# Optimization experiments

Hardware: AMD Instinct MI355X
Metric: run time of the kernel (lower is better)

## Reference

```python
import jax, jax.numpy as jnp
import numpy as np

HEADS = 8
# (src_type, dst_type) for the 8 edge types; node types: 0=op, 1=machine, 2=job
EDGE_DEFS = ((2, 0), (0, 2), (0, 0), (0, 0), (0, 1), (0, 1), (1, 0), (1, 0))
EPS = 1e-5


def _graph_norm(x, gamma, beta):
    # PyG LayerNorm(mode='graph') with batch=None: normalize over ALL nodes and features
    mu = x.mean()
    std = jnp.sqrt(((x - mu) ** 2).mean())
    return (x - mu) / (std + EPS) * gamma + beta


def _hgt_layer(xs, edges, Wkqv, bkqv, krel, vrel, prel, Wout, bout, skip):
    h = xs[0].shape[-1]
    D = h // HEADS
    Ns = [int(x.shape[0]) for x in xs]
    off = np.concatenate([[0], np.cumsum(Ns)])
    Ntot = int(off[-1])
    k, q, v = [], [], []
    for t, x in enumerate(xs):
        kqv = x @ Wkqv[t] + bkqv[t]                    # [N_t, 3h]
        kt, qt, vt = jnp.split(kqv, 3, axis=1)
        k.append(kt.reshape(-1, HEADS, D))
        q.append(qt.reshape(-1, HEADS, D))
        v.append(vt.reshape(-1, HEADS, D))
    alphas, msgs, idxs = [], [], []
    for e, (s, d) in enumerate(EDGE_DEFS):
        src, dst = edges[e][0], edges[e][1]
        # per-edge-type relation transform applied per source node, then gathered per edge
        ke = jnp.einsum('nhd,hde->nhe', k[s], krel[e])[src]   # [E, H, D]
        ve = jnp.einsum('nhd,hde->nhe', v[s], vrel[e])[src]   # [E, H, D]
        qe = q[d][dst]                                        # [E, H, D]
        a = (qe * ke).sum(-1) * prel[e] / jnp.sqrt(jnp.asarray(D, qe.dtype))  # [E, H]
        alphas.append(a)
        msgs.append(ve)
        idxs.append(dst + int(off[d]))
    alpha = jnp.concatenate(alphas, 0)
    msg = jnp.concatenate(msgs, 0)
    idx = jnp.concatenate(idxs, 0)
    # segment softmax over ALL incoming edges per (type-offset) destination node
    amax = jax.ops.segment_max(alpha, idx, num_segments=Ntot)
    ex = jnp.exp(alpha - amax[idx])
    den = jax.ops.segment_sum(ex, idx, num_segments=Ntot)
    w = ex / den[idx]
    agg = jax.ops.segment_sum(msg * w[..., None], idx, num_segments=Ntot).reshape(Ntot, h)
    outs = []
    for t in range(3):
        o = jax.nn.gelu(agg[off[t]:off[t + 1]], approximate=False) @ Wout[t] + bout[t]
        g = jax.nn.sigmoid(skip[t])
        outs.append(g * o + (1.0 - g) * xs[t])
    return outs


def _forward(op_x, machine_x, job_x, W_op, b_op, W_mach, b_mach, W_job, b_job,
             ln_gamma, ln_beta, Wkqv, bkqv, krel, vrel, prel, Wout, bout, skip,
             Wp1, bp1, Wp2, bp2, Wp3, bp3, Wv1, bv1, Wv2, bv2,
             edges, op_idx, m_idx):
    xs = [
        _graph_norm(op_x @ W_op + b_op, ln_gamma[0], ln_beta[0]),
        _graph_norm(machine_x @ W_mach + b_mach, ln_gamma[1], ln_beta[1]),
        _graph_norm(job_x @ W_job + b_job, ln_gamma[2], ln_beta[2]),
    ]
    for l in range(Wkqv.shape[0]):
        xs = _hgt_layer(xs, edges, Wkqv[l], bkqv[l], krel[l], vrel[l], prel[l],
                        Wout[l], bout[l], skip[l])
    op_e, mach_e, job_e = xs
    g = jnp.concatenate([op_e.mean(0), mach_e.mean(0), job_e.mean(0)])  # [3h] global pooled
    value = (jax.nn.relu(g @ Wv1 + bv1) @ Wv2 + bv2)[0]
    P = op_idx.shape[0]
    z = jnp.concatenate([op_e[op_idx], mach_e[m_idx],
                         jnp.broadcast_to(g, (P, g.shape[0]))], axis=1)   # [P, 5h]
    z = jax.nn.relu(z @ Wp1 + bp1)
    z = jax.nn.relu(z @ Wp2 + bp2)
    logits = (z @ Wp3 + bp3)[:, 0]
    return logits, value


def setup_inputs() -> dict:
    key = jax.random.key(0)
    ks = iter(jax.random.split(key, 64))
    NOP, NM, NJ = 50_000, 1_000, 5_000
    H, L, P = 64, 2, 20_000
    D = H // HEADS
    OPF, MF, JF = 8, 7, 7

    def nrm(shape, scale):
        return jax.random.normal(next(ks), shape, jnp.float32) * scale

    def edge(n_src, n_dst, E):
        src = jax.random.randint(next(ks), (E,), 0, n_src, jnp.int32)
        dst = jax.random.randint(next(ks), (E,), 0, n_dst, jnp.int32)
        return jnp.stack([src, dst])

    return {
        'op_x': nrm((NOP, OPF), 1.0),
        'machine_x': nrm((NM, MF), 1.0),
        'job_x': nrm((NJ, JF), 1.0),
        'W_op': nrm((OPF, H), OPF ** -0.5), 'b_op': jnp.zeros((H,), jnp.float32),
        'W_mach': nrm((MF, H), MF ** -0.5), 'b_mach': jnp.zeros((H,), jnp.float32),
        'W_job': nrm((JF, H), JF ** -0.5), 'b_job': jnp.zeros((H,), jnp.float32),
        'ln_gamma': jnp.ones((3, H), jnp.float32), 'ln_beta': jnp.zeros((3, H), jnp.float32),
        'Wkqv': nrm((L, 3, H, 3 * H), H ** -0.5), 'bkqv': jnp.zeros((L, 3, 3 * H), jnp.float32),
        'krel': nrm((L, 8, HEADS, D, D), D ** -0.5), 'vrel': nrm((L, 8, HEADS, D, D), D ** -0.5),
        'prel': jnp.ones((L, 8, HEADS), jnp.float32),
        'Wout': nrm((L, 3, H, H), H ** -0.5), 'bout': jnp.zeros((L, 3, H), jnp.float32),
        'skip': jnp.ones((L, 3), jnp.float32),
        'Wp1': nrm((5 * H, H), (5 * H) ** -0.5), 'bp1': jnp.zeros((H,), jnp.float32),
        'Wp2': nrm((H, H // 2), H ** -0.5), 'bp2': jnp.zeros((H // 2,), jnp.float32),
        'Wp3': nrm((H // 2, 1), (H // 2) ** -0.5), 'bp3': jnp.zeros((1,), jnp.float32),
        'Wv1': nrm((3 * H, H), (3 * H) ** -0.5), 'bv1': jnp.zeros((H,), jnp.float32),
        'Wv2': nrm((H, 1), H ** -0.5), 'bv2': jnp.zeros((1,), jnp.float32),
        'e_contains': edge(NJ, NOP, 50_000),
        'e_belongs': edge(NOP, NJ, 50_000),
        'e_prec': edge(NOP, NOP, 50_000),
        'e_mprec': edge(NOP, NOP, 50_000),
        'e_onmach': edge(NOP, NM, 50_000),
        'e_assign': edge(NOP, NM, 50_000),
        'e_canproc': edge(NM, NOP, 150_000),
        'e_proc': edge(NM, NOP, 50_000),
        'op_idx': jax.random.randint(next(ks), (P,), 0, NOP, jnp.int32),
        'm_idx': jax.random.randint(next(ks), (P,), 0, NM, jnp.int32),
    }


def reference(op_x, machine_x, job_x, W_op, b_op, W_mach, b_mach, W_job, b_job,
              ln_gamma, ln_beta, Wkqv, bkqv, krel, vrel, prel, Wout, bout, skip,
              Wp1, bp1, Wp2, bp2, Wp3, bp3, Wv1, bv1, Wv2, bv2,
              e_contains, e_belongs, e_prec, e_mprec, e_onmach, e_assign,
              e_canproc, e_proc, op_idx, m_idx):
    edges = (e_contains, e_belongs, e_prec, e_mprec, e_onmach, e_assign, e_canproc, e_proc)
    return _forward(op_x, machine_x, job_x, W_op, b_op, W_mach, b_mach, W_job, b_job,
                    ln_gamma, ln_beta, Wkqv, bkqv, krel, vrel, prel, Wout, bout, skip,
                    Wp1, bp1, Wp2, bp2, Wp3, bp3, Wv1, bv1, Wv2, bv2,
                    edges, op_idx, m_idx)
```

## Files before the change

### kernel.cpp

```cpp
#include <hip/hip_runtime.h>


#define KT 32
#define OT 64

__global__ void k_zero2(unsigned int* __restrict__ a, int na,
                        unsigned int* __restrict__ b, int nb) {
    int i = blockIdx.x * 256 + threadIdx.x;
    int st = gridDim.x * 256;
    int tot = na + nb;
    for (; i < tot; i += st) {
        if (i < na) a[i] = 0u; else b[i - na] = 0u;
    }
}

__global__ void k_build(const int* __restrict__ p0, const int* __restrict__ p1,
                        const int* __restrict__ p2, const int* __restrict__ p3,
                        const int* __restrict__ p4, const int* __restrict__ p5,
                        const int* __restrict__ p6, const int* __restrict__ p7,
                        int c1, int c2, int c3, int c4, int c5, int c6, int c7, int c8,
                        int* __restrict__ gkey, int* __restrict__ pack,
                        int* __restrict__ cnt, int fb,
                        const float* __restrict__ op_x, const float* __restrict__ mach_x,
                        const float* __restrict__ job_x,
                        const float* __restrict__ W_op, const float* __restrict__ b_op,
                        const float* __restrict__ W_mach, const float* __restrict__ b_mach,
                        const float* __restrict__ W_job, const float* __restrict__ b_job,
                        float* __restrict__ X, float* __restrict__ nacc,
                        int N0, int N1, int N2) {
    if (blockIdx.x < fb) {
        int g = blockIdx.x * 256 + threadIdx.x;
        if (g >= c8) return;
        const int* ep; int base, E0, et, soff, doff;
        int OJ = N0 + N1;
        if (g < c1)      { ep = p0; base = 0;  E0 = c1 - 0;  et = 0; soff = OJ;  doff = 0;  }
        else if (g < c2) { ep = p1; base = c1; E0 = c2 - c1; et = 1; soff = 0;   doff = OJ; }
        else if (g < c3) { ep = p2; base = c2; E0 = c3 - c2; et = 2; soff = 0;   doff = 0;  }
        else if (g < c4) { ep = p3; base = c3; E0 = c4 - c3; et = 3; soff = 0;   doff = 0;  }
        else if (g < c5) { ep = p4; base = c4; E0 = c5 - c4; et = 4; soff = 0;   doff = N0; }
        else if (g < c6) { ep = p5; base = c5; E0 = c6 - c5; et = 5; soff = 0;   doff = N0; }
        else if (g < c7) { ep = p6; base = c6; E0 = c7 - c6; et = 6; soff = N0;  doff = 0;  }
        else             { ep = p7; base = c7; E0 = c8 - c7; et = 7; soff = N0;  doff = 0;  }
        int i = g - base;
        int kd = (ep[E0 + i] + doff) * 8 + et;
        gkey[g] = kd;
        pack[g] = ep[i] + soff;
        atomicAdd(&cnt[kd], 1);
        return;
    }
    int bid = blockIdx.x - fb;
    int tid = threadIdx.x;
    int j = tid & 63, w = tid >> 6;
    float w0[8], w1[7], w2[7];
    for (int k = 0; k < 8; k++) w0[k] = W_op[k * 64 + j];
    for (int k = 0; k < 7; k++) w1[k] = W_mach[k * 64 + j];
    for (int k = 0; k < 7; k++) w2[k] = W_job[k * 64 + j];
    float b0 = b_op[j], b1 = b_mach[j], b2 = b_job[j];
    float s10 = 0, s20 = 0, s11 = 0, s21 = 0, s12 = 0, s22 = 0;
    int Ntot = N0 + N1 + N2;
    for (int n = bid * 4 + w; n < Ntot; n += 512 * 4) {
        float a;
        if (n < N0) {
            const float* xr = op_x + (size_t)n * 8;
            a = b0;
            for (int k = 0; k < 8; k++) a += xr[k] * w0[k];
            s10 += a; s20 += a * a;
        } else if (n < N0 + N1) {
            const float* xr = mach_x + (size_t)(n - N0) * 7;
            a = b1;
            for (int k = 0; k < 7; k++) a += xr[k] * w1[k];
            s11 += a; s21 += a * a;
        } else {
            const float* xr = job_x + (size_t)(n - N0 - N1) * 7;
            a = b2;
            for (int k = 0; k < 7; k++) a += xr[k] * w2[k];
            s12 += a; s22 += a * a;
        }
        X[(size_t)n * 64 + j] = a;
    }
    for (int o = 32; o > 0; o >>= 1) {
        s10 += __shfl_down(s10, o); s20 += __shfl_down(s20, o);
        s11 += __shfl_down(s11, o); s21 += __shfl_down(s21, o);
        s12 += __shfl_down(s12, o); s22 += __shfl_down(s22, o);
    }
    __shared__ float r[4][6];
    if (j == 0) {
        r[w][0] = s10; r[w][1] = s20; r[w][2] = s11;
        r[w][3] = s21; r[w][4] = s12; r[w][5] = s22;
    }
    __syncthreads();
    if (tid < 6) {
        float v = r[0][tid] + r[1][tid] + r[2][tid] + r[3][tid];
        atomicAdd(&nacc[tid], v);
    }
}

__global__ void k_scan1(const int* __restrict__ cnt, int* __restrict__ partial, int M) {
    __shared__ int s[256];
    int t = threadIdx.x;
    int i = blockIdx.x * 256 + t;
    s[t] = (i < M) ? cnt[i] : 0;
    __syncthreads();
    for (int o = 128; o > 0; o >>= 1) {
        if (t < o) s[t] += s[t + o];
        __syncthreads();
    }
    if (t == 0) partial[blockIdx.x] = s[0];
}

__global__ void k_scan2(const int* __restrict__ cnt, const int* __restrict__ partial,
                        int* __restrict__ rowptr8, int* __restrict__ cursor,
                        int M, int Etot) {
    __shared__ int s[256];
    __shared__ int pbase;
    int t = threadIdx.x;
    int ps = 0;
    for (int c = t; c < blockIdx.x; c += 256) ps += partial[c];
    s[t] = ps;
    __syncthreads();
    for (int o = 128; o > 0; o >>= 1) {
        if (t < o) s[t] += s[t + o];
        __syncthreads();
    }
    if (t == 0) pbase = s[0];
    __syncthreads();
    int base = pbase;
    int i = blockIdx.x * 256 + t;
    int v = (i < M) ? cnt[i] : 0;
    s[t] = v;
    __syncthreads();
    for (int off = 1; off < 256; off <<= 1) {
        int add = (t >= off) ? s[t - off] : 0;
        __syncthreads();
        s[t] += add;
        __syncthreads();
    }
    if (i < M) {
        int r = base + s[t] - v;
        rowptr8[i] = r;
        cursor[i] = r;
    }
    if (blockIdx.x == 0 && t == 0) rowptr8[M] = Etot;
}

__global__ void k_scatter(const int* __restrict__ gkey, const int* __restrict__ pack,
                          int* __restrict__ cursor, int* __restrict__ csr, int Etot) {
    int i = blockIdx.x * 256 + threadIdx.x;
    if (i >= Etot) return;
    int d = gkey[i];
    int pos = atomicAdd(&cursor[d], 1);
    csr[pos] = pack[i];
}

__global__ void k_kqvT(float* __restrict__ X, const float* __restrict__ nacc,
                       const float* __restrict__ ln_gamma, const float* __restrict__ ln_beta,
                       const float* __restrict__ Wl, const float* __restrict__ bl,
                       float* __restrict__ KQV, int tb0, int tb1,
                       int N0, int N1, int N2, int do_norm) {
    __shared__ float Ws[64 * 192];
    __shared__ float Xs[64 * 36];
    __shared__ float Bs[192];
    int b = blockIdx.x;
    int t, nbase, Nt, chunk;
    if (b < tb0)            { t = 0; chunk = b;             nbase = 0;       Nt = N0; }
    else if (b < tb0 + tb1) { t = 1; chunk = b - tb0;       nbase = N0;      Nt = N1; }
    else                    { t = 2; chunk = b - tb0 - tb1; nbase = N0 + N1; Nt = N2; }
    int n0 = nbase + chunk * KT;
    int cntm = nbase + Nt - n0; if (cntm > KT) cntm = KT;

    int tid = threadIdx.x;
    const float* W = Wl + (size_t)t * 64 * 192;
    for (int i = tid; i < 64 * 192; i += 192) Ws[i] = W[i];
    Bs[tid] = bl[t * 192 + tid];

    float mu = 0.0f, sc = 0.0f;
    if (do_norm) {
        float inv = 1.0f / ((float)Nt * 64.0f);
        mu = nacc[2 * t] * inv;
        float var = nacc[2 * t + 1] * inv - mu * mu;
        sc = 1.0f / (sqrtf(fmaxf(var, 0.0f)) + 1e-5f);
    }
    for (int idx = tid; idx < KT * 64; idx += 192) {
        int m = idx >> 6, k = idx & 63;
        float v = 0.0f;
        if (m < cntm) {
            v = X[(size_t)(n0 + m) * 64 + k];
            if (do_norm) {
                v = (v - mu) * sc * ln_gamma[t * 64 + k] + ln_beta[t * 64 + k];
                X[(size_t)(n0 + m) * 64 + k] = v;
            }
        }
        Xs[k * 36 + m] = v;
    }
    __syncthreads();

    int c = tid;
    float bc = Bs[c];
    float acc[KT];
#pragma unroll
    for (int m = 0; m < KT; m++) acc[m] = bc;
    for (int k = 0; k < 64; k++) {
        float wv = Ws[k * 192 + c];
        const float4* xr = (const float4*)(Xs + k * 36);
#pragma unroll
        for (int q = 0; q < KT / 4; q++) {
            float4 x4 = xr[q];
            acc[q * 4 + 0] += x4.x * wv;
            acc[q * 4 + 1] += x4.y * wv;
            acc[q * 4 + 2] += x4.z * wv;
            acc[q * 4 + 3] += x4.w * wv;
        }
    }
    for (int m = 0; m < cntm; m++)
        KQV[(size_t)(n0 + m) * 192 + c] = acc[m];
}

__global__ void k_attnagg(const float* __restrict__ KQV, const int* __restrict__ csr,
                          const int* __restrict__ rowptr8,
                          const float* __restrict__ krel_l, const float* __restrict__ vrel_l,
                          const float* __restrict__ prel_l, float* __restrict__ agg, int Ntot) {
    __shared__ float KRs[8 * 8 * 72];
    __shared__ float VRs[8 * 8 * 72];
    int tid = threadIdx.x;
    for (int i = tid; i < 4096; i += 512) {
        int eth = i >> 6, rest = i & 63;
        KRs[eth * 72 + rest] = krel_l[i] * (prel_l[eth] * 0.35355339059327373f);
        VRs[eth * 72 + rest] = vrel_l[i];
    }
    __syncthreads();

    int j = tid & 63, h = j >> 3, ee = j & 7;
    int wave  = blockIdx.x * 8 + (tid >> 6);
    int nwave = gridDim.x * 8;
    for (int n = wave; n < Ntot; n += nwave) {
        float qv = KQV[(size_t)n * 192 + 64 + j];
        float num = 0.0f, den = 0.0f;
        int e0 = rowptr8[n * 8];
        for (int et = 0; et < 8; et++) {
            int e1 = rowptr8[n * 8 + et + 1];
            if (e0 < e1) {
                const float* KR = KRs + (et * 8 + h) * 72 + ee;
                const float* VR = VRs + (et * 8 + h) * 72 + ee;
                float kr0 = KR[0],  kr1 = KR[8],  kr2 = KR[16], kr3 = KR[24];
                float kr4 = KR[32], kr5 = KR[40], kr6 = KR[48], kr7 = KR[56];
                float vr0 = VR[0],  vr1 = VR[8],  vr2 = VR[16], vr3 = VR[24];
                float vr4 = VR[32], vr5 = VR[40], vr6 = VR[48], vr7 = VR[56];
                int idx = e0;
                for (; idx + 2 <= e1; idx += 2) {
                    int sn0 = csr[idx], sn1 = csr[idx + 1];
                    const float4* ka = (const float4*)(KQV + (size_t)sn0 * 192 + h * 8);
                    const float4* va = (const float4*)(KQV + (size_t)sn0 * 192 + 128 + h * 8);
                    const float4* kb = (const float4*)(KQV + (size_t)sn1 * 192 + h * 8);
                    const float4* vb = (const float4*)(KQV + (size_t)sn1 * 192 + 128 + h * 8);
                    float4 a0 = ka[0], a1 = ka[1], av0 = va[0], av1 = va[1];
                    float4 b0 = kb[0], b1 = kb[1], bv0 = vb[0], bv1 = vb[1];
                    float ke0 = a0.x * kr0 + a0.y * kr1 + a0.z * kr2 + a0.w * kr3
                              + a1.x * kr4 + a1.y * kr5 + a1.z * kr6 + a1.w * kr7;
                    float ve0 = av0.x * vr0 + av0.y * vr1 + av0.z * vr2 + av0.w * vr3
                              + av1.x * vr4 + av1.y * vr5 + av1.z * vr6 + av1.w * vr7;
                    float ke1 = b0.x * kr0 + b0.y * kr1 + b0.z * kr2 + b0.w * kr3
                              + b1.x * kr4 + b1.y * kr5 + b1.z * kr6 + b1.w * kr7;
                    float ve1 = bv0.x * vr0 + bv0.y * vr1 + bv0.z * vr2 + bv0.w * vr3
                              + bv1.x * vr4 + bv1.y * vr5 + bv1.z * vr6 + bv1.w * vr7;
                    float t0 = qv * ke0;
                    t0 += __shfl_xor(t0, 1); t0 += __shfl_xor(t0, 2); t0 += __shfl_xor(t0, 4);
                    float t1 = qv * ke1;
                    t1 += __shfl_xor(t1, 1); t1 += __shfl_xor(t1, 2); t1 += __shfl_xor(t1, 4);
                    float ex0 = __expf(t0);
                    float ex1 = __expf(t1);
                    num += ex0 * ve0 + ex1 * ve1;
                    den += ex0 + ex1;
                }
                if (idx < e1) {
                    int sn = csr[idx];
                    const float4* kr4p = (const float4*)(KQV + (size_t)sn * 192 + h * 8);
                    const float4* vr4p = (const float4*)(KQV + (size_t)sn * 192 + 128 + h * 8);
                    float4 k0 = kr4p[0], k1 = kr4p[1], v0 = vr4p[0], v1 = vr4p[1];
                    float ke = k0.x * kr0 + k0.y * kr1 + k0.z * kr2 + k0.w * kr3
                             + k1.x * kr4 + k1.y * kr5 + k1.z * kr6 + k1.w * kr7;
                    float ve = v0.x * vr0 + v0.y * vr1 + v0.z * vr2 + v0.w * vr3
                             + v1.x * vr4 + v1.y * vr5 + v1.z * vr6 + v1.w * vr7;
                    float tq = qv * ke;
                    tq += __shfl_xor(tq, 1); tq += __shfl_xor(tq, 2); tq += __shfl_xor(tq, 4);
                    float ex = __expf(tq);
                    num += ex * ve;
                    den += ex;
                }
            }
            e0 = e1;
        }
        agg[(size_t)n * 64 + j] = (den > 0.0f) ? (num / den) : 0.0f;
    }
}

__global__ void k_outT(const float* __restrict__ agg, float* __restrict__ X,
                       const float* __restrict__ Wl, const float* __restrict__ bl,
                       const float* __restrict__ skipl, float* __restrict__ gsum,
                       int tb0, int tb1, int N0, int N1, int N2, int do_pool) {
    __shared__ float Ws[64 * 64];
    __shared__ float Gs[64 * 68];
    int b = blockIdx.x;
    int t, nbase, Nt, chunk;
    if (b < tb0)            { t = 0; chunk = b;             nbase = 0;       Nt = N0; }
    else if (b < tb0 + tb1) { t = 1; chunk = b - tb0;       nbase = N0;      Nt = N1; }
    else                    { t = 2; chunk = b - tb0 - tb1; nbase = N0 + N1; Nt = N2; }
    int n0 = nbase + chunk * OT;
    int cntm = nbase + Nt - n0; if (cntm > OT) cntm = OT;

    int tid = threadIdx.x;
    const float* W = Wl + (size_t)t * 64 * 64;
    for (int i = tid; i < 4096; i += 256) Ws[i] = W[i];
    for (int idx = tid; idx < OT * 64; idx += 256) {
        int m = idx >> 6, k = idx & 63;
        float v = 0.0f;
        if (m < cntm) {
            float x = agg[(size_t)(n0 + m) * 64 + k];
            v = 0.5f * x * (1.0f + erff(x * 0.70710678118654752f));
        }
        Gs[k * 68 + m] = v;
    }
    __syncthreads();

    int c = tid & 63, w = tid >> 6;
    float bc = bl[t * 64 + c];
    float gk = 1.0f / (1.0f + __expf(-skipl[t]));
    int m0 = w * 16;
    float acc[16];
#pragma unroll
    for (int i = 0; i < 16; i++) acc[i] = bc;
    for (int k = 0; k < 64; k++) {
        float wv = Ws[k * 64 + c];
        const float4* gr = (const float4*)(Gs + k * 68 + m0);
#pragma unroll
        for (int q = 0; q < 4; q++) {
            float4 g4 = gr[q];
            acc[q * 4 + 0] += g4.x * wv;
            acc[q * 4 + 1] += g4.y * wv;
            acc[q * 4 + 2] += g4.z * wv;
            acc[q * 4 + 3] += g4.w * wv;
        }
    }
    float psum = 0.0f;
    for (int i = 0; i < 16; i++) {
        int m = m0 + i;
        if (m < cntm) {
            float xold = X[(size_t)(n0 + m) * 64 + c];
            float xn = gk * acc[i] + (1.0f - gk) * xold;
            X[(size_t)(n0 + m) * 64 + c] = xn;
            psum += xn;
        }
    }
    if (do_pool) {
        __syncthreads();
        Gs[w * 64 + c] = psum;
        __syncthreads();
        if (tid < 64) {
            float tot = Gs[c] + Gs[64 + c] + Gs[128 + c] + Gs[192 + c];
            atomicAdd(&gsum[t * 64 + c], tot);
        }
    }
}

__global__ void HGTPolicy_53051436040798_kernel(
        const float* __restrict__ X, const float* __restrict__ gsum,
        const int* __restrict__ op_idx, const int* __restrict__ m_idx,
        const float* __restrict__ Wp1, const float* __restrict__ bp1,
        const float* __restrict__ Wp2, const float* __restrict__ bp2,
        const float* __restrict__ Wp3, const float* __restrict__ bp3,
        const float* __restrict__ Wv1, const float* __restrict__ bv1,
        const float* __restrict__ Wv2, const float* __restrict__ bv2,
        float* __restrict__ out, int N0, int N1, int N2, int P, int nb) {
    int tid = threadIdx.x;
    if (blockIdx.x == nb) {
        __shared__ float g[192];
        __shared__ float h1[64];
        int j = tid;
        if (j < 192) {
            float Nd = (j < 64) ? (float)N0 : ((j < 128) ? (float)N1 : (float)N2);
            g[j] = gsum[j] / Nd;
        }
        __syncthreads();
        if (j < 64) {
            float a = bv1[j];
            for (int k = 0; k < 192; k++) a += g[k] * Wv1[k * 64 + j];
            h1[j] = fmaxf(a, 0.0f);
        }
        __syncthreads();
        if (j == 0) {
            float v = bv2[0];
            for (int k = 0; k < 64; k++) v += h1[k] * Wv2[k];
            out[P] = v;
        }
        return;
    }
    __shared__ float z[8][320];
    __shared__ float h1p[8][64];
    __shared__ float h2p[8][32];
    int pp = tid >> 6, j = tid & 63;
    int p = blockIdx.x * 8 + pp;
    int valid = (p < P);
    if (valid) {
        int on = op_idx[p], mn = m_idx[p];
        z[pp][j]       = X[(size_t)on * 64 + j];
        z[pp][64 + j]  = X[(size_t)(N0 + mn) * 64 + j];
        z[pp][128 + j] = gsum[j] / (float)N0;
        z[pp][192 + j] = gsum[64 + j] / (float)N1;
        z[pp][256 + j] = gsum[128 + j] / (float)N2;
    }
    __syncthreads();
    if (valid) {
        const float* zp = z[pp];
        float a = bp1[j];
        for (int k = 0; k < 320; k++) a += zp[k] * Wp1[k * 64 + j];
        h1p[pp][j] = fmaxf(a, 0.0f);
    }
    __syncthreads();
    if (valid && j < 32) {
        const float* hp = h1p[pp];
        float a2 = bp2[j];
        for (int k = 0; k < 64; k++) a2 += hp[k] * Wp2[k * 32 + j];
        h2p[pp][j] = fmaxf(a2, 0.0f);
    }
    __syncthreads();
    if (valid && j == 0) {
        const float* hp = h2p[pp];
        float lg = bp3[0];
        for (int k = 0; k < 32; k++) lg += hp[k] * Wp3[k];
        out[p] = lg;
    }
}

extern "C" void kernel_launch(void* const* d_in, const int* in_sizes, int n_in,
                              void* d_out, int out_size, void* d_ws, size_t ws_size,
                              hipStream_t stream) {
    const float* op_x      = (const float*)d_in[0];
    const float* machine_x = (const float*)d_in[1];
    const float* job_x     = (const float*)d_in[2];
    const float* W_op   = (const float*)d_in[3];
    const float* b_op   = (const float*)d_in[4];
    const float* W_mach = (const float*)d_in[5];
    const float* b_mach = (const float*)d_in[6];
    const float* W_job  = (const float*)d_in[7];
    const float* b_job  = (const float*)d_in[8];
    const float* ln_gamma = (const float*)d_in[9];
    const float* ln_beta  = (const float*)d_in[10];
    const float* Wkqv = (const float*)d_in[11];
    const float* bkqv = (const float*)d_in[12];
    const float* krel = (const float*)d_in[13];
    const float* vrel = (const float*)d_in[14];
    const float* prel = (const float*)d_in[15];
    const float* Wout = (const float*)d_in[16];
    const float* bout = (const float*)d_in[17];
    const float* skip = (const float*)d_in[18];
    const float* Wp1 = (const float*)d_in[19];
    const float* bp1 = (const float*)d_in[20];
    const float* Wp2 = (const float*)d_in[21];
    const float* bp2 = (const float*)d_in[22];
    const float* Wp3 = (const float*)d_in[23];
    const float* bp3 = (const float*)d_in[24];
    const float* Wv1 = (const float*)d_in[25];
    const float* bv1 = (const float*)d_in[26];
    const float* Wv2 = (const float*)d_in[27];
    const float* bv2 = (const float*)d_in[28];
    const int* op_idx = (const int*)d_in[37];
    const int* m_idx  = (const int*)d_in[38];

    const int NOP = in_sizes[0] / 8;
    const int NM  = in_sizes[1] / 7;
    const int NJ  = in_sizes[2] / 7;
    const int L   = in_sizes[11] / (3 * 64 * 192);
    const int P   = in_sizes[37];
    const int Ntot = NOP + NM + NJ;
    const int M = Ntot * 8;

    const int* eptr[8];
    int eoff[9];
    eoff[0] = 0;
    for (int e = 0; e < 8; e++) {
        eptr[e] = (const int*)d_in[29 + e];
        eoff[e + 1] = eoff[e] + in_sizes[29 + e] / 2;
    }
    const int Etot = eoff[8];

    float* ws = (float*)d_ws;
    size_t o = 0;
    float* X    = ws + o; o += (size_t)Ntot * 64;
    float* KQV  = ws + o; o += (size_t)Ntot * 192;
    float* agg  = ws + o; o += (size_t)Ntot * 64;
    float* gsum = ws + o; o += 192;
    float* nacc = ws + o; o += 8;
    int* ib     = (int*)(ws + o);
    size_t io = 0;
    int* cnt     = ib + io; io += M;
    int* rowptr8 = ib + io; io += M + 1;
    int* cursor  = ib + io; io += M;
    int* partial = ib + io; io += 2048;
    int* gkey    = ib + io; io += Etot;
    int* packs   = ib + io; io += Etot;
    int* csr     = ib + io; io += Etot;

    const int kb0 = (NOP + KT - 1) / KT, kb1 = (NM + KT - 1) / KT, kb2 = (NJ + KT - 1) / KT;
    const int kgrid = kb0 + kb1 + kb2;
    const int ob0 = (NOP + OT - 1) / OT, ob1 = (NM + OT - 1) / OT, ob2 = (NJ + OT - 1) / OT;
    const int ogrid = ob0 + ob1 + ob2;
    const int nchunks = (M + 255) / 256;
    const int fb = (Etot + 255) / 256;

    k_zero2<<<256, 256, 0, stream>>>((unsigned int*)cnt, M, (unsigned int*)gsum, 200);

    k_build<<<fb + 512, 256, 0, stream>>>(
        eptr[0], eptr[1], eptr[2], eptr[3], eptr[4], eptr[5], eptr[6], eptr[7],
        eoff[1], eoff[2], eoff[3], eoff[4], eoff[5], eoff[6], eoff[7], eoff[8],
        gkey, packs, cnt, fb,
        op_x, machine_x, job_x, W_op, b_op, W_mach, b_mach, W_job, b_job,
        X, nacc, NOP, NM, NJ);

    k_scan1<<<nchunks, 256, 0, stream>>>(cnt, partial, M);
    k_scan2<<<nchunks, 256, 0, stream>>>(cnt, partial, rowptr8, cursor, M, Etot);
    k_scatter<<<(Etot + 255) / 256, 256, 0, stream>>>(gkey, packs, cursor, csr, Etot);

    for (int l = 0; l < L; l++) {
        k_kqvT<<<kgrid, 192, 0, stream>>>(X, nacc, ln_gamma, ln_beta,
                                          Wkqv + (size_t)l * 3 * 64 * 192,
                                          bkqv + (size_t)l * 3 * 192,
                                          KQV, kb0, kb1, NOP, NM, NJ, (l == 0) ? 1 : 0);
        k_attnagg<<<1024, 512, 0, stream>>>(KQV, csr, rowptr8,
                                            krel + (size_t)l * 4096,
                                            vrel + (size_t)l * 4096,
                                            prel + (size_t)l * 64,
                                            agg, Ntot);
        k_outT<<<ogrid, 256, 0, stream>>>(agg, X,
                                          Wout + (size_t)l * 3 * 64 * 64,
                                          bout + (size_t)l * 3 * 64,
                                          skip + (size_t)l * 3,
                                          gsum, ob0, ob1, NOP, NM, NJ,
                                          (l + 1 == L) ? 1 : 0);
    }

    const int nbP = (P + 7) / 8;
    HGTPolicy_53051436040798_kernel<<<nbP + 1, 512, 0, stream>>>(
        X, gsum, op_idx, m_idx, Wp1, bp1, Wp2, bp2, Wp3, bp3,
        Wv1, bv1, Wv2, bv2, (float*)d_out, NOP, NM, NJ, P, nbP);
}
```

Measured before the change: 674.1 us.

## Fuse CSR scatter with first-layer KQV and merge op-node edge-type loops

The CSR scatter kernel is merged into the first-layer normalize+KQV projection kernel as extra blocks, which removes one launch and lets the two overlap. Edge type is packed into the top byte of each CSR entry. This lets op-destination nodes walk all incoming edges in one combined loop, fetching per-edge relation weights from shared memory instead of looping over eight edge-type segments. The cost is more shared-memory loads per edge on the op path and the assumption that node indices fit in 24 bits.

```diff
diff --git a/kernel.cpp b/kernel.cpp
--- a/kernel.cpp
+++ b/kernel.cpp
@@ -44,7 +44,7 @@
         int i = g - base;
         int kd = (ep[E0 + i] + doff) * 8 + et;
         gkey[g] = kd;
-        pack[g] = ep[i] + soff;
+        pack[g] = (ep[i] + soff) | (et << 24);
         atomicAdd(&cnt[kd], 1);
         return;
     }
@@ -143,24 +143,25 @@
     if (blockIdx.x == 0 && t == 0) rowptr8[M] = Etot;
 }
 
-__global__ void k_scatter(const int* __restrict__ gkey, const int* __restrict__ pack,
-                          int* __restrict__ cursor, int* __restrict__ csr, int Etot) {
-    int i = blockIdx.x * 256 + threadIdx.x;
-    if (i >= Etot) return;
-    int d = gkey[i];
-    int pos = atomicAdd(&cursor[d], 1);
-    csr[pos] = pack[i];
-}
-
-__global__ void k_kqvT(float* __restrict__ X, const float* __restrict__ nacc,
-                       const float* __restrict__ ln_gamma, const float* __restrict__ ln_beta,
-                       const float* __restrict__ Wl, const float* __restrict__ bl,
-                       float* __restrict__ KQV, int tb0, int tb1,
-                       int N0, int N1, int N2, int do_norm) {
+__global__ void k_scatkqv(const int* __restrict__ gkey, const int* __restrict__ pack,
+                          int* __restrict__ cursor, int* __restrict__ csr, int Etot, int sb,
+                          float* __restrict__ X, const float* __restrict__ nacc,
+                          const float* __restrict__ ln_gamma, const float* __restrict__ ln_beta,
+                          const float* __restrict__ Wl, const float* __restrict__ bl,
+                          float* __restrict__ KQV, int tb0, int tb1,
+                          int N0, int N1, int N2) {
     __shared__ float Ws[64 * 192];
     __shared__ float Xs[64 * 36];
     __shared__ float Bs[192];
-    int b = blockIdx.x;
+    if (blockIdx.x < sb) {
+        int i = blockIdx.x * 192 + threadIdx.x;
+        if (i >= Etot) return;
+        int d = gkey[i];
+        int pos = atomicAdd(&cursor[d], 1);
+        csr[pos] = pack[i];
+        return;
+    }
+    int b = blockIdx.x - sb;
     int t, nbase, Nt, chunk;
     if (b < tb0)            { t = 0; chunk = b;             nbase = 0;       Nt = N0; }
     else if (b < tb0 + tb1) { t = 1; chunk = b - tb0;       nbase = N0;      Nt = N1; }
@@ -173,22 +174,17 @@
     for (int i = tid; i < 64 * 192; i += 192) Ws[i] = W[i];
     Bs[tid] = bl[t * 192 + tid];
 
-    float mu = 0.0f, sc = 0.0f;
-    if (do_norm) {
-        float inv = 1.0f / ((float)Nt * 64.0f);
-        mu = nacc[2 * t] * inv;
-        float var = nacc[2 * t + 1] * inv - mu * mu;
-        sc = 1.0f / (sqrtf(fmaxf(var, 0.0f)) + 1e-5f);
-    }
+    float inv = 1.0f / ((float)Nt * 64.0f);
+    float mu = nacc[2 * t] * inv;
+    float var = nacc[2 * t + 1] * inv - mu * mu;
+    float sc = 1.0f / (sqrtf(fmaxf(var, 0.0f)) + 1e-5f);
     for (int idx = tid; idx < KT * 64; idx += 192) {
         int m = idx >> 6, k = idx & 63;
         float v = 0.0f;
         if (m < cntm) {
             v = X[(size_t)(n0 + m) * 64 + k];
-            if (do_norm) {
-                v = (v - mu) * sc * ln_gamma[t * 64 + k] + ln_beta[t * 64 + k];
-                X[(size_t)(n0 + m) * 64 + k] = v;
-            }
+            v = (v - mu) * sc * ln_gamma[t * 64 + k] + ln_beta[t * 64 + k];
+            X[(size_t)(n0 + m) * 64 + k] = v;
         }
         Xs[k * 36 + m] = v;
     }
@@ -215,10 +211,57 @@
         KQV[(size_t)(n0 + m) * 192 + c] = acc[m];
 }
 
+__global__ void k_kqvT(const float* __restrict__ X,
+                       const float* __restrict__ Wl, const float* __restrict__ bl,
+                       float* __restrict__ KQV, int tb0, int tb1,
+                       int N0, int N1, int N2) {
+    __shared__ float Ws[64 * 192];
+    __shared__ float Xs[64 * 36];
+    __shared__ float Bs[192];
+    int b = blockIdx.x;
+    int t, nbase, Nt, chunk;
+    if (b < tb0)            { t = 0; chunk = b;             nbase = 0;       Nt = N0; }
+    else if (b < tb0 + tb1) { t = 1; chunk = b - tb0;       nbase = N0;      Nt = N1; }
+    else                    { t = 2; chunk = b - tb0 - tb1; nbase = N0 + N1; Nt = N2; }
+    int n0 = nbase + chunk * KT;
+    int cntm = nbase + Nt - n0; if (cntm > KT) cntm = KT;
+
+    int tid = threadIdx.x;
+    const float* W = Wl + (size_t)t * 64 * 192;
+    for (int i = tid; i < 64 * 192; i += 192) Ws[i] = W[i];
+    Bs[tid] = bl[t * 192 + tid];
+    for (int idx = tid; idx < KT * 64; idx += 192) {
+        int m = idx >> 6, k = idx & 63;
+        Xs[k * 36 + m] = (m < cntm) ? X[(size_t)(n0 + m) * 64 + k] : 0.0f;
+    }
+    __syncthreads();
+
+    int c = tid;
+    float bc = Bs[c];
+    float acc[KT];
+#pragma unroll
+    for (int m = 0; m < KT; m++) acc[m] = bc;
+    for (int k = 0; k < 64; k++) {
+        float wv = Ws[k * 192 + c];
+        const float4* xr = (const float4*)(Xs + k * 36);
+#pragma unroll
+        for (int q = 0; q < KT / 4; q++) {
+            float4 x4 = xr[q];
+            acc[q * 4 + 0] += x4.x * wv;
+            acc[q * 4 + 1] += x4.y * wv;
+            acc[q * 4 + 2] += x4.z * wv;
+            acc[q * 4 + 3] += x4.w * wv;
+        }
+    }
+    for (int m = 0; m < cntm; m++)
+        KQV[(size_t)(n0 + m) * 192 + c] = acc[m];
+}
+
 __global__ void k_attnagg(const float* __restrict__ KQV, const int* __restrict__ csr,
                           const int* __restrict__ rowptr8,
                           const float* __restrict__ krel_l, const float* __restrict__ vrel_l,
-                          const float* __restrict__ prel_l, float* __restrict__ agg, int Ntot) {
+                          const float* __restrict__ prel_l, float* __restrict__ agg,
+                          int N0, int Ntot) {
     __shared__ float KRs[8 * 8 * 72];
     __shared__ float VRs[8 * 8 * 72];
     int tid = threadIdx.x;
@@ -235,59 +278,114 @@
     for (int n = wave; n < Ntot; n += nwave) {
         float qv = KQV[(size_t)n * 192 + 64 + j];
         float num = 0.0f, den = 0.0f;
-        int e0 = rowptr8[n * 8];
-        for (int et = 0; et < 8; et++) {
-            int e1 = rowptr8[n * 8 + et + 1];
-            if (e0 < e1) {
+        int base8 = n * 8;
+        if (n < N0) {
+            int e0 = rowptr8[base8], e1 = rowptr8[base8 + 8];
+            int idx = e0;
+            for (; idx + 2 <= e1; idx += 2) {
+                int pk0 = csr[idx], pk1 = csr[idx + 1];
+                int sn0 = pk0 & 0xFFFFFF, et0 = ((unsigned int)pk0) >> 24;
+                int sn1 = pk1 & 0xFFFFFF, et1 = ((unsigned int)pk1) >> 24;
+                const float4* ka = (const float4*)(KQV + (size_t)sn0 * 192 + h * 8);
+                const float4* va = (const float4*)(KQV + (size_t)sn0 * 192 + 128 + h * 8);
+                const float4* kb = (const float4*)(KQV + (size_t)sn1 * 192 + h * 8);
+                const float4* vb = (const float4*)(KQV + (size_t)sn1 * 192 + 128 + h * 8);
+                float4 a0 = ka[0], a1 = ka[1], av0 = va[0], av1 = va[1];
+                float4 b0 = kb[0], b1 = kb[1], bv0 = vb[0], bv1 = vb[1];
+                const float* KR0 = KRs + (et0 * 8 + h) * 72 + ee;
+                const float* VR0 = VRs + (et0 * 8 + h) * 72 + ee;
+                const float* KR1 = KRs + (et1 * 8 + h) * 72 + ee;
+                const float* VR1 = VRs + (et1 * 8 + h) * 72 + ee;
+                float ke0 = a0.x * KR0[0]  + a0.y * KR0[8]  + a0.z * KR0[16] + a0.w * KR0[24]
+                          + a1.x * KR0[32] + a1.y * KR0[40] + a1.z * KR0[48] + a1.w * KR0[56];
+                float ve0 = av0.x * VR0[0]  + av0.y * VR0[8]  + av0.z * VR0[16] + av0.w * VR0[24]
+                          + av1.x * VR0[32] + av1.y * VR0[40] + av1.z * VR0[48] + av1.w * VR0[56];
+                float ke1 = b0.x * KR1[0]  + b0.y * KR1[8]  + b0.z * KR1[16] + b0.w * KR1[24]
+                          + b1.x * KR1[32] + b1.y * KR1[40] + b1.z * KR1[48] + b1.w * KR1[56];
+                float ve1 = bv0.x * VR1[0]  + bv0.y * VR1[8]  + bv0.z * VR1[16] + bv0.w * VR1[24]
+                          + bv1.x * VR1[32] + bv1.y * VR1[40] + bv1.z * VR1[48] + bv1.w * VR1[56];
+                float t0 = qv * ke0;
+                t0 += __shfl_xor(t0, 1); t0 += __shfl_xor(t0, 2); t0 += __shfl_xor(t0, 4);
+                float t1 = qv * ke1;
+                t1 += __shfl_xor(t1, 1); t1 += __shfl_xor(t1, 2); t1 += __shfl_xor(t1, 4);
+                float ex0 = __expf(t0);
+                float ex1 = __expf(t1);
+                num += ex0 * ve0 + ex1 * ve1;
+                den += ex0 + ex1;
+            }
+            if (idx < e1) {
+                int pk = csr[idx];
+                int sn = pk & 0xFFFFFF, et = ((unsigned int)pk) >> 24;
+                const float4* kr4 = (const float4*)(KQV + (size_t)sn * 192 + h * 8);
+                const float4* vr4 = (const float4*)(KQV + (size_t)sn * 192 + 128 + h * 8);
+                float4 k0 = kr4[0], k1 = kr4[1], v0 = vr4[0], v1 = vr4[1];
                 const float* KR = KRs + (et * 8 + h) * 72 + ee;
                 const float* VR = VRs + (et * 8 + h) * 72 + ee;
-                float kr0 = KR[0],  kr1 = KR[8],  kr2 = KR[16], kr3 = KR[24];
-                float kr4 = KR[32], kr5 = KR[40], kr6 = KR[48], kr7 = KR[56];
-                float vr0 = VR[0],  vr1 = VR[8],  vr2 = VR[16], vr3 = VR[24];
-                float vr4 = VR[32], vr5 = VR[40], vr6 = VR[48], vr7 = VR[56];
-                int idx = e0;
-                for (; idx + 2 <= e1; idx += 2) {
-                    int sn0 = csr[idx], sn1 = csr[idx + 1];
-                    const float4* ka = (const float4*)(KQV + (size_t)sn0 * 192 + h * 8);
-                    const float4* va = (const float4*)(KQV + (size_t)sn0 * 192 + 128 + h * 8);
-                    const float4* kb = (const float4*)(KQV + (size_t)sn1 * 192 + h * 8);
-                    const float4* vb = (const float4*)(KQV + (size_t)sn1 * 192 + 128 + h * 8);
-                    float4 a0 = ka[0], a1 = ka[1], av0 = va[0], av1 = va[1];
-                    float4 b0 = kb[0], b1 = kb[1], bv0 = vb[0], bv1 = vb[1];
-                    float ke0 = a0.x * kr0 + a0.y * kr1 + a0.z * kr2 + a0.w * kr3
-                              + a1.x * kr4 + a1.y * kr5 + a1.z * kr6 + a1.w * kr7;
-                    float ve0 = av0.x * vr0 + av0.y * vr1 + av0.z * vr2 + av0.w * vr3
-                              + av1.x * vr4 + av1.y * vr5 + av1.z * vr6 + av1.w * vr7;
-                    float ke1 = b0.x * kr0 + b0.y * kr1 + b0.z * kr2 + b0.w * kr3
-                              + b1.x * kr4 + b1.y * kr5 + b1.z * kr6 + b1.w * kr7;
-                    float ve1 = bv0.x * vr0 + bv0.y * vr1 + bv0.z * vr2 + bv0.w * vr3
-                              + bv1.x * vr4 + bv1.y * vr5 + bv1.z * vr6 + bv1.w * vr7;
-                    float t0 = qv * ke0;
-                    t0 += __shfl_xor(t0, 1); t0 += __shfl_xor(t0, 2); t0 += __shfl_xor(t0, 4);
-                    float t1 = qv * ke1;
-                    t1 += __shfl_xor(t1, 1); t1 += __shfl_xor(t1, 2); t1 += __shfl_xor(t1, 4);
-                    float ex0 = __expf(t0);
-                    float ex1 = __expf(t1);
-                    num += ex0 * ve0 + ex1 * ve1;
-                    den += ex0 + ex1;
+                float ke = k0.x * KR[0]  + k0.y * KR[8]  + k0.z * KR[16] + k0.w * KR[24]
+                         + k1.x * KR[32] + k1.y * KR[40] + k1.z * KR[48] + k1.w * KR[56];
+                float ve = v0.x * VR[0]  + v0.y * VR[8]  + v0.z * VR[16] + v0.w * VR[24]
+                         + v1.x * VR[32] + v1.y * VR[40] + v1.z * VR[48] + v1.w * VR[56];
+                float tq = qv * ke;
+                tq += __shfl_xor(tq, 1); tq += __shfl_xor(tq, 2); tq += __shfl_xor(tq, 4);
+                float ex = __expf(tq);
+                num += ex * ve;
+                den += ex;
+            }
+        } else {
+            int e0 = rowptr8[base8];
+            for (int et = 0; et < 8; et++) {
+                int e1 = rowptr8[base8 + et + 1];
+                if (e0 < e1) {
+                    const float* KR = KRs + (et * 8 + h) * 72 + ee;
+                    const float* VR = VRs + (et * 8 + h) * 72 + ee;
+                    float kr0 = KR[0],  kr1 = KR[8],  kr2 = KR[16], kr3 = KR[24];
+                    float kr4 = KR[32], kr5 = KR[40], kr6 = KR[48], kr7 = KR[56];
+                    float vq0 = VR[0],  vq1 = VR[8],  vq2 = VR[16], vq3 = VR[24];
+                    float vq4 = VR[32], vq5 = VR[40], vq6 = VR[48], vq7 = VR[56];
+                    int idx = e0;
+                    for (; idx + 2 <= e1; idx += 2) {
+                        int sn0 = csr[idx] & 0xFFFFFF, sn1 = csr[idx + 1] & 0xFFFFFF;
+                        const float4* ka = (const float4*)(KQV + (size_t)sn0 * 192 + h * 8);
+                        const float4* va = (const float4*)(KQV + (size_t)sn0 * 192 + 128 + h * 8);
+                        const float4* kb = (const float4*)(KQV + (size_t)sn1 * 192 + h * 8);
+                        const float4* vb = (const float4*)(KQV + (size_t)sn1 * 192 + 128 + h * 8);
+                        float4 a0 = ka[0], a1 = ka[1], av0 = va[0], av1 = va[1];
+                        float4 b0 = kb[0], b1 = kb[1], bv0 = vb[0], bv1 = vb[1];
+                        float ke0 = a0.x * kr0 + a0.y * kr1 + a0.z * kr2 + a0.w * kr3
+                                  + a1.x * kr4 + a1.y * kr5 + a1.z * kr6 + a1.w * kr7;
+                        float ve0 = av0.x * vq0 + av0.y * vq1 + av0.z * vq2 + av0.w * vq3
+                                  + av1.x * vq4 + av1.y * vq5 + av1.z * vq6 + av1.w * vq7;
+                        float ke1 = b0.x * kr0 + b0.y * kr1 + b0.z * kr2 + b0.w * kr3
+                                  + b1.x * kr4 + b1.y * kr5 + b1.z * kr6 + b1.w * kr7;
+                        float ve1 = bv0.x * vq0 + bv0.y * vq1 + bv0.z * vq2 + bv0.w * vq3
+                                  + bv1.x * vq4 + bv1.y * vq5 + bv1.z * vq6 + bv1.w * vq7;
+                        float t0 = qv * ke0;
+                        t0 += __shfl_xor(t0, 1); t0 += __shfl_xor(t0, 2); t0 += __shfl_xor(t0, 4);
+                        float t1 = qv * ke1;
+                        t1 += __shfl_xor(t1, 1); t1 += __shfl_xor(t1, 2); t1 += __shfl_xor(t1, 4);
+                        float ex0 = __expf(t0);
+                        float ex1 = __expf(t1);
+                        num += ex0 * ve0 + ex1 * ve1;
+                        den += ex0 + ex1;
+                    }
+                    if (idx < e1) {
+                        int sn = csr[idx] & 0xFFFFFF;
+                        const float4* kp = (const float4*)(KQV + (size_t)sn * 192 + h * 8);
+                        const float4* vp = (const float4*)(KQV + (size_t)sn * 192 + 128 + h * 8);
+                        float4 k0 = kp[0], k1 = kp[1], v0 = vp[0], v1 = vp[1];
+                        float ke = k0.x * kr0 + k0.y * kr1 + k0.z * kr2 + k0.w * kr3
+                                 + k1.x * kr4 + k1.y * kr5 + k1.z * kr6 + k1.w * kr7;
+                        float ve = v0.x * vq0 + v0.y * vq1 + v0.z * vq2 + v0.w * vq3
+                                 + v1.x * vq4 + v1.y * vq5 + v1.z * vq6 + v1.w * vq7;
+                        float tq = qv * ke;
+                        tq += __shfl_xor(tq, 1); tq += __shfl_xor(tq, 2); tq += __shfl_xor(tq, 4);
+                        float ex = __expf(tq);
+                        num += ex * ve;
+                        den += ex;
+                    }
                 }
-                if (idx < e1) {
-                    int sn = csr[idx];
-                    const float4* kr4p = (const float4*)(KQV + (size_t)sn * 192 + h * 8);
-                    const float4* vr4p = (const float4*)(KQV + (size_t)sn * 192 + 128 + h * 8);
-                    float4 k0 = kr4p[0], k1 = kr4p[1], v0 = vr4p[0], v1 = vr4p[1];
-                    float ke = k0.x * kr0 + k0.y * kr1 + k0.z * kr2 + k0.w * kr3
-                             + k1.x * kr4 + k1.y * kr5 + k1.z * kr6 + k1.w * kr7;
-                    float ve = v0.x * vr0 + v0.y * vr1 + v0.z * vr2 + v0.w * vr3
-                             + v1.x * vr4 + v1.y * vr5 + v1.z * vr6 + v1.w * vr7;
-                    float tq = qv * ke;
-                    tq += __shfl_xor(tq, 1); tq += __shfl_xor(tq, 2); tq += __shfl_xor(tq, 4);
-                    float ex = __expf(tq);
-                    num += ex * ve;
-                    den += ex;
-                }
+                e0 = e1;
             }
-            e0 = e1;
         }
         agg[(size_t)n * 64 + j] = (den > 0.0f) ? (num / den) : 0.0f;
     }
@@ -505,6 +603,7 @@
     const int ogrid = ob0 + ob1 + ob2;
     const int nchunks = (M + 255) / 256;
     const int fb = (Etot + 255) / 256;
+    const int sb = (Etot + 191) / 192;
 
     k_zero2<<<256, 256, 0, stream>>>((unsigned int*)cnt, M, (unsigned int*)gsum, 200);
 
@@ -517,18 +616,23 @@
 
     k_scan1<<<nchunks, 256, 0, stream>>>(cnt, partial, M);
     k_scan2<<<nchunks, 256, 0, stream>>>(cnt, partial, rowptr8, cursor, M, Etot);
-    k_scatter<<<(Etot + 255) / 256, 256, 0, stream>>>(gkey, packs, cursor, csr, Etot);
+
+    k_scatkqv<<<sb + kgrid, 192, 0, stream>>>(gkey, packs, cursor, csr, Etot, sb,
+                                              X, nacc, ln_gamma, ln_beta,
+                                              Wkqv, bkqv, KQV, kb0, kb1, NOP, NM, NJ);
 
     for (int l = 0; l < L; l++) {
-        k_kqvT<<<kgrid, 192, 0, stream>>>(X, nacc, ln_gamma, ln_beta,
-                                          Wkqv + (size_t)l * 3 * 64 * 192,
-                                          bkqv + (size_t)l * 3 * 192,
-                                          KQV, kb0, kb1, NOP, NM, NJ, (l == 0) ? 1 : 0);
+        if (l > 0) {
+            k_kqvT<<<kgrid, 192, 0, stream>>>(X,
+                                              Wkqv + (size_t)l * 3 * 64 * 192,
+                                              bkqv + (size_t)l * 3 * 192,
+                                              KQV, kb0, kb1, NOP, NM, NJ);
+        }
         k_attnagg<<<1024, 512, 0, stream>>>(KQV, csr, rowptr8,
                                             krel + (size_t)l * 4096,
                                             vrel + (size_t)l * 4096,
                                             prel + (size_t)l * 64,
-                                            agg, Ntot);
+                                            agg, NOP, Ntot);
         k_outT<<<ogrid, 256, 0, stream>>>(agg, X,
                                           Wout + (size_t)l * 3 * 64 * 64,
                                           bout + (size_t)l * 3 * 64,
```

New measurement: 640.9 us (median of 2 runs). 4.9% less time.
